# Optimization experiments

Measured on AMD Instinct MI355X. Metric: run time of the kernel, lower is better.

Reference implementation:

```python
import jax, jax.numpy as jnp
import numpy as np

B, S, D, H = 4, 2048, 1024, 16
HD = D // H  # head_dim = 64


def setup_inputs() -> dict:
    key = jax.random.key(0)
    k1, k2, k3, k4, k5 = jax.random.split(key, 5)
    x = jax.random.normal(k1, (B, S, D), dtype=jnp.float32)
    # per-head QKV projection weights (H separate Linear(D, 3*HD) layers, batched)
    Wqkv = jax.random.normal(k2, (H, D, 3 * HD), dtype=jnp.float32) * (D ** -0.5)
    bqkv = jax.random.normal(k3, (H, 3 * HD), dtype=jnp.float32) * 0.02
    # output projection Linear(D, D)
    Wo = jax.random.normal(k4, (D, D), dtype=jnp.float32) * (D ** -0.5)
    bo = jax.random.normal(k5, (D,), dtype=jnp.float32) * 0.02
    return {"x": x, "Wqkv": Wqkv, "bqkv": bqkv, "Wo": Wo, "bo": bo}


def reference(x, Wqkv, bqkv, Wo, bo):
    # Batched per-head QKV projection: [B,S,D] x [H,D,3*HD] -> [B,H,S,3*HD]
    qkv = jnp.einsum('bsd,hde->bhse', x, Wqkv) + bqkv[None, :, None, :]
    q, k, v = jnp.split(qkv, 3, axis=-1)  # each [B,H,S,HD]
    scale = HD ** -0.5
    scores = jnp.einsum('bhqe,bhke->bhqk', q, k) * scale  # [B,H,S,S]
    causal = jnp.tril(jnp.ones((S, S), dtype=bool))
    scores = jnp.where(causal, scores, -jnp.inf)
    attn = jax.nn.softmax(scores, axis=-1)
    # dropout is identity in eval mode
    out = jnp.einsum('bhqk,bhke->bhqe', attn, v)  # [B,H,S,HD]
    out = jnp.transpose(out, (0, 2, 1, 3)).reshape(B, S, D)  # concat heads
    return out @ Wo + bo
```

## Files before the change

### kernel.cpp

```cpp
#include <hip/hip_runtime.h>
#include <hip/hip_bf16.h>

#define B_ 4
#define S_ 2048
#define D_ 1024
#define H_ 16
#define HD_ 64
#define M_TOK 8192
#define QSCALE 0.18033688f

typedef __attribute__((ext_vector_type(4))) float f32x4;
typedef __attribute__((ext_vector_type(8))) short short8;
typedef __attribute__((ext_vector_type(4))) short short4_t;

__device__ inline short f2bf(float f) {
  unsigned u = __builtin_bit_cast(unsigned, f);
  u += 0x7fff + ((u >> 16) & 1);
  return (short)(u >> 16);
}
__device__ inline short f2bf_trunc(float f) {
  return (short)(__builtin_bit_cast(unsigned, f) >> 16);
}

typedef __attribute__((address_space(1))) const unsigned int gas_u32;
typedef __attribute__((address_space(3))) unsigned int las_u32;
__device__ inline void gload_lds16(const void* g, void* l) {
  __builtin_amdgcn_global_load_lds((gas_u32*)g, (las_u32*)l, 16, 0, 0);
}


__global__ __launch_bounds__(256) void conv_x_kernel(
    const float* __restrict__ x, short* __restrict__ xb) {
  size_t base = ((size_t)blockIdx.x * 256 + threadIdx.x) * 8;
  f32x4 v0 = *reinterpret_cast<const f32x4*>(&x[base]);
  f32x4 v1 = *reinterpret_cast<const f32x4*>(&x[base + 4]);
  short8 o;
  o[0]=f2bf(v0[0]); o[1]=f2bf(v0[1]); o[2]=f2bf(v0[2]); o[3]=f2bf(v0[3]);
  o[4]=f2bf(v1[0]); o[5]=f2bf(v1[1]); o[6]=f2bf(v1[2]); o[7]=f2bf(v1[3]);
  *reinterpret_cast<short8*>(&xb[base]) = o;
}

__global__ __launch_bounds__(256) void conv_wqkv_kernel(
    const float* __restrict__ Wqkv, short* __restrict__ wqkvt) {
  const int h = blockIdx.x;
  const int k0 = blockIdx.y * 32;
  const int tid = threadIdx.x;
  __shared__ short T[192 * 40];
#pragma unroll
  for (int i = 0; i < 6; ++i) {
    int iv = tid + i * 256;
    int k = iv / 48;
    int e4 = (iv % 48) * 4;
    f32x4 v = *reinterpret_cast<const f32x4*>(&Wqkv[((size_t)h * D_ + k0 + k) * 192 + e4]);
#pragma unroll
    for (int j = 0; j < 4; ++j) T[(e4 + j) * 40 + k] = f2bf(v[j]);
  }
  __syncthreads();
#pragma unroll
  for (int i = 0; i < 6; ++i) {
    int iv = tid + i * 256;
    int e = iv >> 3;
    int g4 = iv & 7;
    short4_t o = *reinterpret_cast<const short4_t*>(&T[e * 40 + g4 * 4]);
    *reinterpret_cast<short4_t*>(&wqkvt[(size_t)(h * 192 + e) * 1024 + k0 + g4 * 4]) = o;
  }
}

__global__ __launch_bounds__(256) void conv_wo_kernel(
    const float* __restrict__ Wo, short* __restrict__ wot) {
  const int k0 = blockIdx.x * 32;
  const int n0 = blockIdx.y * 128;
  const int tid = threadIdx.x;
  __shared__ short T[128 * 40];
#pragma unroll
  for (int i = 0; i < 4; ++i) {
    int iv = tid + i * 256;
    int k = iv >> 5;
    int n4 = (iv & 31) * 4;
    f32x4 v = *reinterpret_cast<const f32x4*>(&Wo[(size_t)(k0 + k) * 1024 + n0 + n4]);
#pragma unroll
    for (int j = 0; j < 4; ++j) T[(n4 + j) * 40 + k] = f2bf(v[j]);
  }
  __syncthreads();
#pragma unroll
  for (int i = 0; i < 4; ++i) {
    int iv = tid + i * 256;
    int e = iv >> 3;
    int g4 = iv & 7;
    short4_t o = *reinterpret_cast<const short4_t*>(&T[e * 40 + g4 * 4]);
    *reinterpret_cast<short4_t*>(&wot[(size_t)(n0 + e) * 1024 + k0 + g4 * 4]) = o;
  }
}

template<int EPI>
__global__ __launch_bounds__(256) void gemm_kernel(
    const short* __restrict__ A, const short* __restrict__ Bt,
    const float* __restrict__ bias,
    short* __restrict__ qb, short* __restrict__ kb, short* __restrict__ vt,
    float* __restrict__ out) {
  const int m0 = blockIdx.x * 128;
  const int n0 = blockIdx.y * 128;
  const int tid = threadIdx.x;
  const int lane = tid & 63, wv = tid >> 6;
  const int wr = wv >> 1, wc = wv & 1;
  const int g = lane >> 4, c = lane & 15;

  __shared__ short As[128 * 32];
  __shared__ short Bs[128 * 32];

  const f32x4 zero4 = {0.f, 0.f, 0.f, 0.f};
  f32x4 acc[4][4];
#pragma unroll
  for (int i = 0; i < 4; ++i)
#pragma unroll
    for (int j = 0; j < 4; ++j) acc[i][j] = zero4;

  const int row_l = tid >> 2;
  const int chunk = tid & 3;
  const short* ga = A  + (size_t)(m0 + row_l) * D_ + chunk * 8;
  const short* gb = Bt + (size_t)(n0 + row_l) * D_ + chunk * 8;
  char* lA = (char*)As + tid * 16;
  char* lB = (char*)Bs + tid * 16;

  for (int k0 = 0; k0 < D_; k0 += 32) {
    gload_lds16(ga + k0,            lA);
    gload_lds16(ga + 64 * D_ + k0,  lA + 4096);
    gload_lds16(gb + k0,            lB);
    gload_lds16(gb + 64 * D_ + k0,  lB + 4096);
    asm volatile("s_waitcnt vmcnt(0)" ::: "memory");
    __syncthreads();
    short8 a[4], b[4];
#pragma unroll
    for (int t = 0; t < 4; ++t) {
      a[t] = *reinterpret_cast<const short8*>(&As[(wr * 64 + t * 16 + c) * 32 + g * 8]);
      b[t] = *reinterpret_cast<const short8*>(&Bs[(wc * 64 + t * 16 + c) * 32 + g * 8]);
    }
#pragma unroll
    for (int mt = 0; mt < 4; ++mt)
#pragma unroll
      for (int nt = 0; nt < 4; ++nt)
        acc[mt][nt] = __builtin_amdgcn_mfma_f32_16x16x32_bf16(a[mt], b[nt], acc[mt][nt], 0, 0, 0);
    __syncthreads();
  }

#pragma unroll
  for (int mt = 0; mt < 4; ++mt) {
#pragma unroll
    for (int nt = 0; nt < 4; ++nt) {
      int n = n0 + wc * 64 + nt * 16 + c;
      float bv = bias[n];
      int m_base = m0 + wr * 64 + mt * 16 + g * 4;
      if (EPI == 0) {
        int h = n / 192, e = n % 192;
        int bb2 = m_base >> 11, s0 = m_base & 2047;
        size_t plane = (size_t)(bb2 * H_ + h) * (S_ * HD_);
        if (e < 64) {
          size_t bp = plane + (size_t)(s0 >> 4) * 1024 + (e >> 3) * 128 + (s0 & 15) * 8 + (e & 7);
#pragma unroll
          for (int r = 0; r < 4; ++r)
            qb[bp + r * 8] = f2bf((acc[mt][nt][r] + bv) * QSCALE);
        } else if (e < 128) {
          int ek = e - 64;
          size_t bp = plane + (size_t)(s0 >> 4) * 1024 + (ek >> 3) * 128 + (s0 & 15) * 8 + (ek & 7);
#pragma unroll
          for (int r = 0; r < 4; ++r)
            kb[bp + r * 8] = f2bf(acc[mt][nt][r] + bv);
        } else {
          int hd = e - 128;
          size_t bp = plane + (size_t)((hd >> 4) * 64 + (s0 >> 5)) * 512 +
                      ((s0 >> 3) & 3) * 128 + (hd & 15) * 8 + (s0 & 7);
          short4_t vv;
#pragma unroll
          for (int r = 0; r < 4; ++r) vv[r] = f2bf(acc[mt][nt][r] + bv);
          *reinterpret_cast<short4_t*>(&vt[bp]) = vv;
        }
      } else {
#pragma unroll
        for (int r = 0; r < 4; ++r)
          out[(size_t)(m_base + r) * D_ + n] = acc[mt][nt][r] + bv;
      }
    }
  }
}

struct KF32 { short8 f[4]; };

__device__ __forceinline__ void load_kf32(KF32& k, const short* __restrict__ kbh,
                                          int ktb, int lane) {
#pragma unroll
  for (int cc = 0; cc < 2; ++cc)
#pragma unroll
    for (int t = 0; t < 2; ++t)
      k.f[cc * 2 + t] = *reinterpret_cast<const short8*>(
          &kbh[(size_t)(ktb * 2 + t) * 1024 + cc * 512 + lane * 8]);
}

__global__ __launch_bounds__(256, 3) void attn_kernel(
    const short* __restrict__ qb, const short* __restrict__ kb,
    const short* __restrict__ vt, short* __restrict__ av) {
  const int orig = blockIdx.x;
  const int xcd = orig & 7;
  const int local = orig >> 3;
  const int bh = xcd * 8 + (local & 7);
  const int qt = 15 - (local >> 3);
  const int bb = bh >> 4, h = bh & 15;
  const int tid = threadIdx.x;
  const int lane = tid & 63, wv = tid >> 6;
  const int g = lane >> 4, c = lane & 15;
  const int q0 = qt * 128;
  const int r0 = q0 + wv * 32;

  __shared__ short Ps[4][32 * 40];
  short* Pw = Ps[wv];

  const short* qbh = qb + (size_t)bh * S_ * HD_;
  const short* kbh = kb + (size_t)bh * S_ * HD_;
  const short* vth = vt + (size_t)bh * HD_ * S_;

  short8 ones;
#pragma unroll
  for (int j = 0; j < 8; ++j) ones[j] = (short)0x3F80;

  const f32x4 zero4 = {0.f, 0.f, 0.f, 0.f};

  short8 qf[2][2];
#pragma unroll
  for (int mt = 0; mt < 2; ++mt)
#pragma unroll
    for (int cc = 0; cc < 2; ++cc)
      qf[mt][cc] = *reinterpret_cast<const short8*>(
          &qbh[(size_t)(r0 / 16 + mt) * 1024 + cc * 512 + lane * 8]);

  f32x4 acc_o[2][4];
  f32x4 lacc[2];
#pragma unroll
  for (int mt = 0; mt < 2; ++mt) {
    lacc[mt] = zero4;
#pragma unroll
    for (int nt = 0; nt < 4; ++nt) acc_o[mt][nt] = zero4;
  }

  const int diag = 4 * qt + wv;
  const int nk = diag + 1;

  KF32 kA, kB;
  load_kf32(kA, kbh, 0, lane);

  auto body = [&](int ktb, KF32& kc, KF32& kn) {
    const int k0 = ktb * 32;
    short8 vf[4];
#pragma unroll
    for (int nt = 0; nt < 4; ++nt)
      vf[nt] = *reinterpret_cast<const short8*>(
          &vth[(size_t)(nt * 64 + ktb) * 512 + lane * 8]);
    f32x4 sc[2][2];
#pragma unroll
    for (int mt = 0; mt < 2; ++mt)
#pragma unroll
      for (int t = 0; t < 2; ++t) sc[mt][t] = zero4;
#pragma unroll
    for (int cc = 0; cc < 2; ++cc)
#pragma unroll
      for (int mt = 0; mt < 2; ++mt)
#pragma unroll
        for (int t = 0; t < 2; ++t)
          sc[mt][t] = __builtin_amdgcn_mfma_f32_16x16x32_bf16(
              qf[mt][cc], kc.f[cc * 2 + t], sc[mt][t], 0, 0, 0);
    int ktbn = ktb + 1;
    if (ktbn >= S_ / 32) ktbn = 0;
    load_kf32(kn, kbh, ktbn, lane);
    if (ktb == diag) {
#pragma unroll
      for (int mt = 0; mt < 2; ++mt)
#pragma unroll
        for (int t = 0; t < 2; ++t) {
          const int key = k0 + t * 16 + c;
#pragma unroll
          for (int r = 0; r < 4; ++r) {
            const int qi = r0 + mt * 16 + g * 4 + r;
            if (key > qi) sc[mt][t][r] = -INFINITY;
          }
        }
    }
#pragma unroll
    for (int mt = 0; mt < 2; ++mt)
#pragma unroll
      for (int t = 0; t < 2; ++t)
#pragma unroll
        for (int r = 0; r < 4; ++r) {
          float pf = __builtin_exp2f(sc[mt][t][r]);
          Pw[(mt * 16 + g * 4 + r) * 40 + t * 16 + c] = f2bf_trunc(pf);
        }
    short8 pa[2];
#pragma unroll
    for (int mt = 0; mt < 2; ++mt)
      pa[mt] = *reinterpret_cast<const short8*>(&Pw[(mt * 16 + c) * 40 + g * 8]);
#pragma unroll
    for (int mt = 0; mt < 2; ++mt)
      lacc[mt] = __builtin_amdgcn_mfma_f32_16x16x32_bf16(pa[mt], ones, lacc[mt], 0, 0, 0);
#pragma unroll
    for (int mt = 0; mt < 2; ++mt)
#pragma unroll
      for (int nt = 0; nt < 4; ++nt)
        acc_o[mt][nt] = __builtin_amdgcn_mfma_f32_16x16x32_bf16(
            pa[mt], vf[nt], acc_o[mt][nt], 0, 0, 0);
  };

  int ktb = 0;
  for (; ktb + 1 < nk; ktb += 2) {
    body(ktb,     kA, kB);
    body(ktb + 1, kB, kA);
  }
  if (ktb < nk) body(ktb, kA, kB);

#pragma unroll
  for (int mt = 0; mt < 2; ++mt) {
    float inv[4];
#pragma unroll
    for (int r = 0; r < 4; ++r) inv[r] = 1.0f / lacc[mt][r];
#pragma unroll
    for (int nt = 0; nt < 4; ++nt)
#pragma unroll
      for (int r = 0; r < 4; ++r) {
        int R = r0 + mt * 16 + g * 4 + r;
        av[(size_t)(bb * S_ + R) * D_ + h * HD_ + nt * 16 + c] =
            f2bf(acc_o[mt][nt][r] * inv[r]);
      }
  }
}

extern "C" void kernel_launch(void* const* d_in, const int* in_sizes, int n_in,
                              void* d_out, int out_size, void* d_ws, size_t ws_size,
                              hipStream_t stream) {
  const float* x    = (const float*)d_in[0];
  const float* Wqkv = (const float*)d_in[1];
  const float* bqkv = (const float*)d_in[2];
  const float* Wo   = (const float*)d_in[3];
  const float* bo   = (const float*)d_in[4];
  float* out = (float*)d_out;

  const size_t NTOK = (size_t)B_ * H_ * S_ * HD_;
  short* xb    = (short*)d_ws;
  short* wqkvt = xb + (size_t)M_TOK * D_;
  short* wot   = wqkvt + (size_t)3072 * 1024;
  short* qb    = wot + (size_t)1024 * 1024;
  short* kb    = qb + NTOK;
  short* vt    = kb + NTOK;
  short* av    = xb;

  conv_x_kernel   <<<4096, 256, 0, stream>>>(x, xb);
  conv_wqkv_kernel<<<dim3(16, 32), 256, 0, stream>>>(Wqkv, wqkvt);
  conv_wo_kernel  <<<dim3(32, 8), 256, 0, stream>>>(Wo, wot);
  gemm_kernel<0>  <<<dim3(64, 24), 256, 0, stream>>>(xb, wqkvt, bqkv, qb, kb, vt, nullptr);
  attn_kernel     <<<1024, 256, 0, stream>>>(qb, kb, vt, av);
  gemm_kernel<1>  <<<dim3(64, 8), 256, 0, stream>>>(av, wot, bo, nullptr, nullptr, nullptr, out);
}
```

Before: 183.3 us.

## Rewrite projection GEMMs with triple-buffered swizzled LDS pipeline and XCD-aware tiling

Replaces the simple single-buffered 128x128 GEMM with a 256x128-tile, 512-thread kernel that prefetches two K-tiles ahead into a three-slot LDS ring using async global-to-LDS loads. It adds an XOR swizzle on LDS rows to avoid bank conflicts, a K-step of 64, raised MFMA priority, and a block-to-tile mapping that groups N tiles per XCD to improve L2 reuse. The aim is to hide global load latency behind MFMA work and cut the per-iteration full sync stalls. The cost is a large LDS footprint (144KB) that limits occupancy, plus more complex indexing in the epilogue path.

```diff
diff --git a/kernel.cpp b/kernel.cpp
--- a/kernel.cpp
+++ b/kernel.cpp
@@ -27,7 +27,6 @@
 __device__ inline void gload_lds16(const void* g, void* l) {
   __builtin_amdgcn_global_load_lds((gas_u32*)g, (las_u32*)l, 16, 0, 0);
 }
-
 
 __global__ __launch_bounds__(256) void conv_x_kernel(
     const float* __restrict__ x, short* __restrict__ xb) {
@@ -92,21 +91,29 @@
   }
 }
 
-template<int EPI>
-__global__ __launch_bounds__(256) void gemm_kernel(
+template<int EPI, int N_>
+__global__ __launch_bounds__(512, 2) void gemm2_kernel(
     const short* __restrict__ A, const short* __restrict__ Bt,
     const float* __restrict__ bias,
     short* __restrict__ qb, short* __restrict__ kb, short* __restrict__ vt,
     float* __restrict__ out) {
-  const int m0 = blockIdx.x * 128;
-  const int n0 = blockIdx.y * 128;
+  constexpr int KD = 1024;
+  constexpr int NT = N_ / 128;
+  constexpr int MT = 32;
+  constexpr int NKT = KD / 64;
+  const int bid = blockIdx.x;
+  const int xcd = bid & 7;
+  const int idx = bid >> 3;
+  const int n_t = xcd * (NT / 8) + idx / MT;
+  const int m_t = idx & (MT - 1);
+  const int m0 = m_t * 256, n0 = n_t * 128;
+
   const int tid = threadIdx.x;
   const int lane = tid & 63, wv = tid >> 6;
-  const int wr = wv >> 1, wc = wv & 1;
+  const int wm = wv >> 1, wn = wv & 1;
   const int g = lane >> 4, c = lane & 15;
 
-  __shared__ short As[128 * 32];
-  __shared__ short Bs[128 * 32];
+  __shared__ short lds_pool[73728];
 
   const f32x4 zero4 = {0.f, 0.f, 0.f, 0.f};
   f32x4 acc[4][4];
@@ -115,41 +122,76 @@
 #pragma unroll
     for (int j = 0; j < 4; ++j) acc[i][j] = zero4;
 
-  const int row_l = tid >> 2;
-  const int chunk = tid & 3;
-  const short* ga = A  + (size_t)(m0 + row_l) * D_ + chunk * 8;
-  const short* gb = Bt + (size_t)(n0 + row_l) * D_ + chunk * 8;
-  char* lA = (char*)As + tid * 16;
-  char* lB = (char*)Bs + tid * 16;
-
-  for (int k0 = 0; k0 < D_; k0 += 32) {
-    gload_lds16(ga + k0,            lA);
-    gload_lds16(ga + 64 * D_ + k0,  lA + 4096);
-    gload_lds16(gb + k0,            lB);
-    gload_lds16(gb + 64 * D_ + k0,  lB + 4096);
-    asm volatile("s_waitcnt vmcnt(0)" ::: "memory");
-    __syncthreads();
-    short8 a[4], b[4];
-#pragma unroll
-    for (int t = 0; t < 4; ++t) {
-      a[t] = *reinterpret_cast<const short8*>(&As[(wr * 64 + t * 16 + c) * 32 + g * 8]);
-      b[t] = *reinterpret_cast<const short8*>(&Bs[(wc * 64 + t * 16 + c) * 32 + g * 8]);
-    }
-#pragma unroll
-    for (int mt = 0; mt < 4; ++mt)
+  auto STAGE = [&](int kt, int buf) {
+    const short* asrc = A + (size_t)m0 * KD + kt * 64;
+#pragma unroll
+    for (int i = 0; i < 4; ++i) {
+      int ch = tid + i * 512;
+      int row = ch >> 3;
+      int slot = (ch & 7) ^ (row & 7);
+      gload_lds16(asrc + (size_t)row * KD + slot * 8,
+                  &lds_pool[buf * 16384 + ch * 8]);
+    }
+    const short* bsrc = Bt + (size_t)n0 * KD + kt * 64;
+#pragma unroll
+    for (int i = 0; i < 2; ++i) {
+      int ch = tid + i * 512;
+      int row = ch >> 3;
+      int slot = (ch & 7) ^ (row & 7);
+      gload_lds16(bsrc + (size_t)row * KD + slot * 8,
+                  &lds_pool[49152 + buf * 8192 + ch * 8]);
+    }
+  };
+
+  STAGE(0, 0);
+  STAGE(1, 1);
+  int cb = 0;
+
+  const int xs = (c & 7) << 4;
+  const int xk0 = ((g * 16) ^ xs) >> 1;
+  const int xk1 = ((64 + g * 16) ^ xs) >> 1;
+
+  for (int t = 0; t < NKT; ++t) {
+    __builtin_amdgcn_sched_barrier(0);
+    __builtin_amdgcn_s_barrier();
+    __builtin_amdgcn_sched_barrier(0);
+    const int kt = (t + 2 < NKT) ? t + 2 : NKT - 1;
+    const int sb = (cb + 2 >= 3) ? cb - 1 : cb + 2;
+    STAGE(kt, sb);
+    asm volatile("s_waitcnt vmcnt(12)" ::: "memory");
+    __builtin_amdgcn_s_barrier();
+    __builtin_amdgcn_sched_barrier(0);
+
+    const short* Ab = &lds_pool[cb * 16384];
+    const short* Bb = &lds_pool[49152 + cb * 8192];
+#pragma unroll
+    for (int kh = 0; kh < 2; ++kh) {
+      const int xk = kh ? xk1 : xk0;
+      short8 a[4], b[4];
+#pragma unroll
+      for (int mt = 0; mt < 4; ++mt)
+        a[mt] = *reinterpret_cast<const short8*>(&Ab[(wm * 64 + mt * 16 + c) * 64 + xk]);
 #pragma unroll
       for (int nt = 0; nt < 4; ++nt)
-        acc[mt][nt] = __builtin_amdgcn_mfma_f32_16x16x32_bf16(a[mt], b[nt], acc[mt][nt], 0, 0, 0);
-    __syncthreads();
+        b[nt] = *reinterpret_cast<const short8*>(&Bb[(wn * 64 + nt * 16 + c) * 64 + xk]);
+      __builtin_amdgcn_s_setprio(1);
+#pragma unroll
+      for (int mt = 0; mt < 4; ++mt)
+#pragma unroll
+        for (int nt = 0; nt < 4; ++nt)
+          acc[mt][nt] = __builtin_amdgcn_mfma_f32_16x16x32_bf16(a[mt], b[nt], acc[mt][nt], 0, 0, 0);
+      __builtin_amdgcn_s_setprio(0);
+    }
+    cb = (cb + 1 == 3) ? 0 : cb + 1;
   }
 
 #pragma unroll
   for (int mt = 0; mt < 4; ++mt) {
 #pragma unroll
     for (int nt = 0; nt < 4; ++nt) {
-      int n = n0 + wc * 64 + nt * 16 + c;
+      int n = n0 + wn * 64 + nt * 16 + c;
       float bv = bias[n];
-      int m_base = m0 + wr * 64 + mt * 16 + g * 4;
+      int m_base = m0 + wm * 64 + mt * 16 + g * 4;
       if (EPI == 0) {
         int h = n / 192, e = n % 192;
         int bb2 = m_base >> 11, s0 = m_base & 2047;
@@ -351,7 +393,7 @@
   conv_x_kernel   <<<4096, 256, 0, stream>>>(x, xb);
   conv_wqkv_kernel<<<dim3(16, 32), 256, 0, stream>>>(Wqkv, wqkvt);
   conv_wo_kernel  <<<dim3(32, 8), 256, 0, stream>>>(Wo, wot);
-  gemm_kernel<0>  <<<dim3(64, 24), 256, 0, stream>>>(xb, wqkvt, bqkv, qb, kb, vt, nullptr);
+  gemm2_kernel<0, 3072><<<768, 512, 0, stream>>>(xb, wqkvt, bqkv, qb, kb, vt, nullptr);
   attn_kernel     <<<1024, 256, 0, stream>>>(qb, kb, vt, av);
-  gemm_kernel<1>  <<<dim3(64, 8), 256, 0, stream>>>(av, wot, bo, nullptr, nullptr, nullptr, out);
-}
+  gemm2_kernel<1, 1024><<<256, 512, 0, stream>>>(av, wot, bo, nullptr, nullptr, nullptr, out);
+}
```

Result: no change. 186.9 us (+2.0%).

## Triple-buffer GEMM LDS tiles with async prefetch and XOR-swizzled layout

Applied to the files above, without the earlier changes.

Replaces the single-buffered GEMM main loop, which waited for each K-tile load before computing, with a 3-stage ring of LDS buffers. Tile t+2 is prefetched while tile t is computed, using partial vmcnt waits so global loads overlap MFMA work. The global-to-LDS addressing is XOR-swizzled to cut LDS bank conflicts, and s_setprio is raised around the MFMA block. It also sets a minimum of 3 blocks per CU in launch bounds. The cost is more LDS per block, which can limit occupancy, plus more complex synchronization that must be exactly right.

```diff
diff --git a/kernel.cpp b/kernel.cpp
--- a/kernel.cpp
+++ b/kernel.cpp
@@ -27,7 +27,6 @@
 __device__ inline void gload_lds16(const void* g, void* l) {
   __builtin_amdgcn_global_load_lds((gas_u32*)g, (las_u32*)l, 16, 0, 0);
 }
-
 
 __global__ __launch_bounds__(256) void conv_x_kernel(
     const float* __restrict__ x, short* __restrict__ xb) {
@@ -93,11 +92,13 @@
 }
 
 template<int EPI>
-__global__ __launch_bounds__(256) void gemm_kernel(
+__global__ __launch_bounds__(256, 3) void gemm3_kernel(
     const short* __restrict__ A, const short* __restrict__ Bt,
     const float* __restrict__ bias,
     short* __restrict__ qb, short* __restrict__ kb, short* __restrict__ vt,
     float* __restrict__ out) {
+  constexpr int KD = 1024;
+  constexpr int NKT = KD / 32;
   const int m0 = blockIdx.x * 128;
   const int n0 = blockIdx.y * 128;
   const int tid = threadIdx.x;
@@ -105,8 +106,7 @@
   const int wr = wv >> 1, wc = wv & 1;
   const int g = lane >> 4, c = lane & 15;
 
-  __shared__ short As[128 * 32];
-  __shared__ short Bs[128 * 32];
+  __shared__ short lds_pool[24576];
 
   const f32x4 zero4 = {0.f, 0.f, 0.f, 0.f};
   f32x4 acc[4][4];
@@ -115,32 +115,66 @@
 #pragma unroll
     for (int j = 0; j < 4; ++j) acc[i][j] = zero4;
 
-  const int row_l = tid >> 2;
-  const int chunk = tid & 3;
-  const short* ga = A  + (size_t)(m0 + row_l) * D_ + chunk * 8;
-  const short* gb = Bt + (size_t)(n0 + row_l) * D_ + chunk * 8;
-  char* lA = (char*)As + tid * 16;
-  char* lB = (char*)Bs + tid * 16;
-
-  for (int k0 = 0; k0 < D_; k0 += 32) {
-    gload_lds16(ga + k0,            lA);
-    gload_lds16(ga + 64 * D_ + k0,  lA + 4096);
-    gload_lds16(gb + k0,            lB);
-    gload_lds16(gb + 64 * D_ + k0,  lB + 4096);
-    asm volatile("s_waitcnt vmcnt(0)" ::: "memory");
-    __syncthreads();
+  auto STAGE = [&](int kt, int buf) {
+    const short* asrc = A + (size_t)m0 * KD + kt * 32;
+#pragma unroll
+    for (int i = 0; i < 2; ++i) {
+      int ch = tid + i * 256;
+      int row = ch >> 2;
+      int slot = (ch & 3) ^ ((row >> 1) & 3);
+      gload_lds16(asrc + (size_t)row * KD + slot * 8,
+                  &lds_pool[buf * 4096 + ch * 8]);
+    }
+    const short* bsrc = Bt + (size_t)n0 * KD + kt * 32;
+#pragma unroll
+    for (int i = 0; i < 2; ++i) {
+      int ch = tid + i * 256;
+      int row = ch >> 2;
+      int slot = (ch & 3) ^ ((row >> 1) & 3);
+      gload_lds16(bsrc + (size_t)row * KD + slot * 8,
+                  &lds_pool[12288 + buf * 4096 + ch * 8]);
+    }
+  };
+
+  STAGE(0, 0);
+  STAGE(1, 1);
+  int cb = 0;
+
+  const int sread = (g ^ ((c >> 1) & 3)) * 8;
+
+  for (int t = 0; t < NKT; ++t) {
+    __builtin_amdgcn_sched_barrier(0);
+    __builtin_amdgcn_s_barrier();
+    __builtin_amdgcn_sched_barrier(0);
+    if (t + 2 < NKT) {
+      int sb = (cb + 2 >= 3) ? cb - 1 : cb + 2;
+      STAGE(t + 2, sb);
+      asm volatile("s_waitcnt vmcnt(8)" ::: "memory");
+    } else if (t + 1 < NKT) {
+      asm volatile("s_waitcnt vmcnt(4)" ::: "memory");
+    } else {
+      asm volatile("s_waitcnt vmcnt(0)" ::: "memory");
+    }
+    __builtin_amdgcn_s_barrier();
+    __builtin_amdgcn_sched_barrier(0);
+
+    const short* Ab = &lds_pool[cb * 4096];
+    const short* Bb = &lds_pool[12288 + cb * 4096];
     short8 a[4], b[4];
 #pragma unroll
-    for (int t = 0; t < 4; ++t) {
-      a[t] = *reinterpret_cast<const short8*>(&As[(wr * 64 + t * 16 + c) * 32 + g * 8]);
-      b[t] = *reinterpret_cast<const short8*>(&Bs[(wc * 64 + t * 16 + c) * 32 + g * 8]);
-    }
+    for (int mt = 0; mt < 4; ++mt)
+      a[mt] = *reinterpret_cast<const short8*>(&Ab[(wr * 64 + mt * 16 + c) * 32 + sread]);
+#pragma unroll
+    for (int nt = 0; nt < 4; ++nt)
+      b[nt] = *reinterpret_cast<const short8*>(&Bb[(wc * 64 + nt * 16 + c) * 32 + sread]);
+    __builtin_amdgcn_s_setprio(1);
 #pragma unroll
     for (int mt = 0; mt < 4; ++mt)
 #pragma unroll
       for (int nt = 0; nt < 4; ++nt)
         acc[mt][nt] = __builtin_amdgcn_mfma_f32_16x16x32_bf16(a[mt], b[nt], acc[mt][nt], 0, 0, 0);
-    __syncthreads();
+    __builtin_amdgcn_s_setprio(0);
+    cb = (cb + 1 == 3) ? 0 : cb + 1;
   }
 
 #pragma unroll
@@ -351,7 +385,7 @@
   conv_x_kernel   <<<4096, 256, 0, stream>>>(x, xb);
   conv_wqkv_kernel<<<dim3(16, 32), 256, 0, stream>>>(Wqkv, wqkvt);
   conv_wo_kernel  <<<dim3(32, 8), 256, 0, stream>>>(Wo, wot);
-  gemm_kernel<0>  <<<dim3(64, 24), 256, 0, stream>>>(xb, wqkvt, bqkv, qb, kb, vt, nullptr);
+  gemm3_kernel<0> <<<dim3(64, 24), 256, 0, stream>>>(xb, wqkvt, bqkv, qb, kb, vt, nullptr);
   attn_kernel     <<<1024, 256, 0, stream>>>(qb, kb, vt, av);
-  gemm_kernel<1>  <<<dim3(64, 8), 256, 0, stream>>>(av, wot, bo, nullptr, nullptr, nullptr, out);
-}
+  gemm3_kernel<1> <<<dim3(64, 8), 256, 0, stream>>>(av, wot, bo, nullptr, nullptr, nullptr, out);
+}
```

Measured after the change: 168.0 us. -8.4%, faster.
